# Kernel tuning notes

Hardware: AMD Instinct MI355X
Metric: run time of the kernel (lower is better)

Reference implementation:

```python
import jax, jax.numpy as jnp
import numpy as np

# SLAYER neuron / simulation constants (netParams)
THETA = 10.0      # spike threshold
TS = 1.0          # simulation timestep (ms)
TAU_SR = 10.0     # PSP (srm) time constant
TAU_REF = 1.0     # refractory time constant
SCALE_REF = 2.0   # refractory strength (in units of theta)
TAU_RHO = 1.0     # surrogate-gradient width
SCALE_RHO = 1.0   # surrogate-gradient scale
DECAY_SR = float(np.exp(-TS / TAU_SR))
DECAY_REF = float(np.exp(-TS / TAU_REF))


def psp(x):
    """Leaky-integrate PSP filter over time. x: (N, F, T) -> (N, F, T)."""
    xt = jnp.moveaxis(x, -1, 0)  # (T, N, F)
    def step(p, s):
        p = DECAY_SR * p + s
        return p, p
    _, ps = jax.lax.scan(step, jnp.zeros_like(xt[0]), xt)
    return jnp.moveaxis(ps, 0, -1)


@jax.custom_vjp
def heaviside(v):
    return (v >= 0).astype(v.dtype)

def _h_fwd(v):
    return heaviside(v), v

def _h_bwd(v, g):
    # SLAYER-style fast-sigmoid/exponential surrogate gradient
    return (g * SCALE_RHO * jnp.exp(-jnp.abs(v) / TAU_RHO),)

heaviside.defvjp(_h_fwd, _h_bwd)


def spike(u):
    """Threshold membrane potential with leaky refractory feedback.
    u: (N, F, T) -> binary spikes (N, F, T)."""
    ut = jnp.moveaxis(u, -1, 0)  # (T, N, F)
    def step(r, u_t):
        v = u_t + r                       # membrane + refractory state
        s = heaviside(v - THETA)
        r_next = DECAY_REF * (r - SCALE_REF * THETA * s)
        return r_next, s
    _, ss = jax.lax.scan(step, jnp.zeros_like(ut[0]), ut)
    return jnp.moveaxis(ss, 0, -1)


def dense(w, x):
    """Per-timestep linear layer. w: (O, F), x: (N, F, T) -> (N, O, T)."""
    return jnp.einsum('of,nft->not', w, x)


def setup_inputs() -> dict:
    key = jax.random.key(0)
    k1, k2, k3, k4, k5, k6 = jax.random.split(key, 6)
    N, T = 16, 500
    # binary spike inputs (float32 for differentiability through psp)
    xt = (jax.random.uniform(k1, (N, 156, T)) < 0.10).astype(jnp.float32)
    xv = (jax.random.uniform(k2, (N, 6300, T)) < 0.02).astype(jnp.float32)
    # dense weights (scaled so membrane potentials can cross theta=10)
    Wt = jax.random.normal(k3, (50, 156), jnp.float32) * (4.0 / np.sqrt(156))
    Wv1 = jax.random.normal(k4, (1024, 6300), jnp.float32) * (4.0 / np.sqrt(6300))
    Wv2 = jax.random.normal(k5, (10, 1024), jnp.float32) * (4.0 / np.sqrt(1024))
    Wf = jax.random.normal(k6, (20, 60), jnp.float32) * (4.0 / np.sqrt(60))
    return {"spikeInputTact": xt, "spikeInputVis": xv,
            "Wt": Wt, "Wv1": Wv1, "Wv2": Wv2, "Wf": Wf}


def reference(spikeInputTact, spikeInputVis, Wt, Wv1, Wv2, Wf):
    # tactile encoder: spike(fc1(psp(x)))
    s_tact = spike(dense(Wt, psp(spikeInputTact)))          # (N, 50, T)
    # vision encoder: two slayer dense+psp+spike stages
    sv1 = spike(dense(Wv1, psp(spikeInputVis)))             # (N, 1024, T)
    s_vis = spike(dense(Wv2, psp(sv1)))                     # (N, 10, T)
    # fuse and classify: spike(psp(fc1(cat)))
    s_all = jnp.concatenate([s_tact, s_vis], axis=1)        # (N, 60, T)
    out = spike(psp(dense(Wf, s_all)))                      # (N, 20, T)
    return out
```

## Files before the change

kernel.cpp:

```cpp
#include <hip/hip_runtime.h>
#include <stdint.h>

#define DSR   0.90483741803595952f
#define DREF  0.36787944117144233f
#define THETA 10.0f
#define REFAMP 20.0f

#define NB 16
#define TT 500
#define TP 512
#define F1 6300
#define KP 6400
#define NKS 50
#define O1 1024
#define NC 8192
#define FT 156
#define OT 50
#define O2 10
#define OF 20

typedef __attribute__((ext_vector_type(4)))  float f32x4;
typedef __attribute__((ext_vector_type(4)))  int   i32x4;
typedef __attribute__((ext_vector_type(16))) int   i32x16;

#define GLL16(g, l) __builtin_amdgcn_global_load_lds( \
    (const __attribute__((address_space(1))) void*)(g), \
    (__attribute__((address_space(3))) void*)(l), 16, 0, 0)

__global__ void __launch_bounds__(512) k_prep(const float* __restrict__ xv,
                                              const float* __restrict__ W,
                                              unsigned char* __restrict__ Bg,
                                              char* __restrict__ H0,
                                              char* __restrict__ H1) {
  __shared__ unsigned char tb[64][516];
  int bx = blockIdx.x, tid = threadIdx.x;
  if (bx < 1600) {
    int ft = bx % 100, n = bx / 100;
    int f0 = ft * 64;
    int ks = ft >> 1, half = ft & 1;
#pragma unroll
    for (int it = 0; it < 16; ++it) {
      int idx = it * 512 + tid;
      int row = idx >> 7, c4 = idx & 127;
      int f = f0 + row, t = c4 * 4;
      uchar4 b = make_uchar4(0, 0, 0, 0);
      if (f < F1) {
        if (t + 3 < TT) {
          f32x4 v = *(const f32x4*)(xv + ((size_t)n * F1 + f) * TT + t);
          b.x = (v[0] != 0.f); b.y = (v[1] != 0.f);
          b.z = (v[2] != 0.f); b.w = (v[3] != 0.f);
        } else {
#pragma unroll
          for (int j = 0; j < 4; ++j)
            if (t + j < TT) {
              float v = xv[((size_t)n * F1 + f) * TT + t + j];
              ((unsigned char*)&b)[j] = (v != 0.f);
            }
        }
      }
      *(uchar4*)&tb[row][t] = b;
    }
    __syncthreads();
    int lane = tid & 63, w = tid >> 6;
#pragma unroll 8
    for (int i = 0; i < 64; ++i) {
      int tl = w * 64 + i;
      unsigned long long mask = __ballot(tb[lane][tl] != 0);
      if (lane == 0) {
        unsigned lo = (unsigned)mask, hi = (unsigned)(mask >> 32);
        unsigned w0 = __builtin_amdgcn_perm(hi, lo, 0x05040100u);
        unsigned w1 = __builtin_amdgcn_perm(hi, lo, 0x07060302u);
        int col = n * TP + tl;
        unsigned char* g = Bg + ((size_t)ks * 8192 + col) * 16 + half * 4;
        *(unsigned*)(g) = w0;
        *(unsigned*)(g + 8) = w1;
      }
    }
  } else {
    int sb = bx - 1600;
    int o0 = sb * 4;
#pragma unroll
    for (int it = 0; it < 13; ++it) {
      int e = it * 2048 + tid * 4;
      if (e < 25600) {
        int row = e / 6400;
        int f = e - row * 6400;
        int o = o0 + row;
        float w4[4] = {0.f, 0.f, 0.f, 0.f};
        if (f < F1) {
          const f32x4 v = *(const f32x4*)(W + (size_t)o * F1 + f);
          w4[0] = v[0]; w4[1] = v[1]; w4[2] = v[2]; w4[3] = v[3];
        }
        char c0[4], c1[4];
#pragma unroll
        for (int j = 0; j < 4; ++j) {
          int wq = __float2int_rn(w4[j] * 32768.0f);
          int h0 = ((wq + 128) & 255) - 128;
          int h1 = (wq - h0) >> 8;
          c0[j] = (char)h0; c1[j] = (char)h1;
        }
        *(char4*)(H0 + (size_t)o * KP + f) = make_char4(c0[0], c0[1], c0[2], c0[3]);
        *(char4*)(H1 + (size_t)o * KP + f) = make_char4(c1[0], c1[1], c1[2], c1[3]);
      }
    }
  }
}

__global__ void __launch_bounds__(512) k_tact(const float* __restrict__ xt,
                                              const float* __restrict__ Wt,
                                              float* __restrict__ s_tact) {
  __shared__ float atv[TP * 26];
  int n = blockIdx.x >> 1, half = blockIdx.x & 1;
  int t = threadIdx.x;
  if (t < TT) {
    float acc[25];
#pragma unroll
    for (int o = 0; o < 25; ++o) acc[o] = 0.f;
    for (int f = 0; f < FT; ++f) {
      float x = xt[((size_t)n * FT + f) * TT + t];
#pragma unroll
      for (int o = 0; o < 25; ++o)
        acc[o] = fmaf(Wt[(half * 25 + o) * FT + f], x, acc[o]);
    }
#pragma unroll
    for (int o = 0; o < 25; ++o) atv[t * 26 + o] = acc[o];
  }
  __syncthreads();
  if (t < 25) {
    float p = 0.f, r = 0.f;
    float* op = s_tact + ((size_t)n * OT + half * 25 + t) * TT;
    for (int i = 0; i < TT; i += 10) {
      float u[10];
#pragma unroll
      for (int j = 0; j < 10; ++j) u[j] = atv[(i + j) * 26 + t];
#pragma unroll
      for (int j = 0; j < 10; ++j) {
        p = DSR * p + u[j];
        float v = p + r;
        bool s = (v >= THETA);
        r = DREF * (r - (s ? REFAMP : 0.f));
        op[i + j] = s ? 1.f : 0.f;
      }
    }
  }
}

__global__ void __launch_bounds__(512, 4) k_gemm(const char* __restrict__ H0,
                                                 const char* __restrict__ H1,
                                                 const unsigned char* __restrict__ Bg,
                                                 float* __restrict__ C) {
  __shared__ char A0[2][128 * 128];
  __shared__ char A1[2][128 * 128];
  int tid = threadIdx.x, bid = blockIdx.x;
  int gy = bid & 7, gx = bid >> 3;
  int wave = tid >> 6, lane = tid & 63;
  int wr = wave >> 1, wc = wave & 1;
  int l31 = lane & 31, h = lane >> 5;

  i32x16 acc0[2], acc1[2];
#pragma unroll
  for (int nn = 0; nn < 2; ++nn) { acc0[nn] = (i32x16)0; acc1[nn] = (i32x16)0; }

  size_t ga[2]; unsigned ldsa[2];
#pragma unroll
  for (int j = 0; j < 2; ++j) {
    int p = j * 512 + tid;
    int row = p >> 3;
    int src = (p & 7) ^ (row & 7);
    ga[j] = (size_t)(gy * 128 + row) * KP + src * 16;
    ldsa[j] = (unsigned)p * 16u;
  }
  const unsigned char* bp[2];
#pragma unroll
  for (int nn = 0; nn < 2; ++nn)
    bp[nn] = Bg + ((size_t)(gx * 128 + wc * 64 + nn * 32 + l31) * 16) + h * 8;

  int ra = wr * 32 + l31;
  int offA[4];
#pragma unroll
  for (int kk = 0; kk < 4; ++kk)
    offA[kk] = ra * 128 + (((kk * 2 + h) ^ (ra & 7)) * 16);

#define STAGE(ks, buf) do {                                       \
    size_t ko = (size_t)(ks) * 128;                               \
    GLL16(H0 + ga[0] + ko, (char*)&A0[buf][0] + ldsa[0]);         \
    GLL16(H0 + ga[1] + ko, (char*)&A0[buf][0] + ldsa[1]);         \
    GLL16(H1 + ga[0] + ko, (char*)&A1[buf][0] + ldsa[0]);         \
    GLL16(H1 + ga[1] + ko, (char*)&A1[buf][0] + ldsa[1]);         \
  } while (0)

#define LDB(ks, arr) do {                                         \
    _Pragma("unroll")                                             \
    for (int nn = 0; nn < 2; ++nn)                                \
      arr[nn] = *(const uint2*)(bp[nn] + (size_t)(ks) * 131072);  \
  } while (0)

#define BODY(ks, buf, bregs) do {                                               \
    if ((ks) == NKS - 1) { asm volatile("s_waitcnt vmcnt(0)" ::: "memory"); }   \
    else                 { asm volatile("s_waitcnt vmcnt(6)" ::: "memory"); }   \
    __builtin_amdgcn_sched_barrier(0);                                          \
    __builtin_amdgcn_s_barrier();                                               \
    __builtin_amdgcn_sched_barrier(0);                                          \
    _Pragma("unroll")                                                           \
    for (int kk = 0; kk < 4; ++kk) {                                            \
      i32x4 fa0 = *(const i32x4*)(&A0[buf][0] + offA[kk]);                      \
      i32x4 fa1 = *(const i32x4*)(&A1[buf][0] + offA[kk]);                      \
      i32x4 bv[2];                                                              \
      _Pragma("unroll")                                                         \
      for (int nn = 0; nn < 2; ++nn) {                                          \
        unsigned x = ((kk < 2) ? bregs[nn].x : bregs[nn].y) >> ((kk & 1) * 16); \
        x &= 0xFFFFu;                                                           \
        _Pragma("unroll")                                                       \
        for (int w = 0; w < 4; ++w) {                                           \
          unsigned nib = (x >> (4 * w)) & 0xFu;                                 \
          bv[nn][w] = (int)((nib * 0x00204081u) & 0x01010101u);                 \
        }                                                                       \
      }                                                                         \
      __builtin_amdgcn_s_setprio(1);                                            \
      _Pragma("unroll")                                                         \
      for (int nn = 0; nn < 2; ++nn) {                                          \
        acc0[nn] = __builtin_amdgcn_mfma_i32_32x32x32_i8(fa0, bv[nn], acc0[nn], 0, 0, 0); \
        acc1[nn] = __builtin_amdgcn_mfma_i32_32x32x32_i8(fa1, bv[nn], acc1[nn], 0, 0, 0); \
      }                                                                         \
      __builtin_amdgcn_s_setprio(0);                                            \
    }                                                                           \
    __builtin_amdgcn_s_barrier();                                               \
    __builtin_amdgcn_sched_barrier(0);                                          \
    if ((ks) + 2 < NKS) { STAGE((ks) + 2, buf); LDB((ks) + 2, bregs); }         \
  } while (0)

  uint2 bA[2], bB[2];
  STAGE(0, 0); LDB(0, bA);
  STAGE(1, 1); LDB(1, bB);

  for (int ks = 0; ks < NKS; ks += 2) {
    BODY(ks, 0, bA);
    BODY(ks + 1, 1, bB);
  }
#undef BODY
#undef LDB
#undef STAGE

#pragma unroll
  for (int nn = 0; nn < 2; ++nn) {
    int ob = gy * 128 + wr * 32;
    int cb = gx * 128 + wc * 64 + nn * 32 + l31;
#pragma unroll
    for (int reg = 0; reg < 16; ++reg) {
      int row = (reg & 3) + 8 * (reg >> 2) + 4 * h;
      int v = acc0[nn][reg] + (acc1[nn][reg] << 8);
      C[(size_t)(ob + row) * NC + cb] = (float)v * (1.0f / 32768.0f);
    }
  }
}

__global__ void __launch_bounds__(256) k_spk1(const float* __restrict__ C,
                                              const float* __restrict__ Wv2,
                                              float* __restrict__ a2part) {
  __shared__ float tile[128 * 65];
  __shared__ char  spkb[128 * 68];
  __shared__ float w2s[O2][64];
  int og = blockIdx.x, n = blockIdx.y;
  int tid = threadIdx.x;
  for (int i = tid; i < O2 * 64; i += 256)
    w2s[i >> 6][i & 63] = Wv2[(i >> 6) * O1 + og * 64 + (i & 63)];
  float p = 0.f, r = 0.f;
  for (int tc = 0; tc < 4; ++tc) {
#pragma unroll
    for (int i = 0; i < 8; ++i) {
      int idx = i * 256 + tid;
      int row = idx >> 5, c4 = idx & 31;
      f32x4 v = *(const f32x4*)(C + (size_t)(og * 64 + row) * NC + n * TP + tc * 128 + c4 * 4);
#pragma unroll
      for (int j = 0; j < 4; ++j) tile[(c4 * 4 + j) * 65 + row] = v[j];
    }
    __syncthreads();
    if (tid < 64) {
      float pp = p, rr = r;
      for (int i = 0; i < 128; i += 8) {
        float u[8];
#pragma unroll
        for (int j = 0; j < 8; ++j) u[j] = tile[(i + j) * 65 + tid];
#pragma unroll
        for (int j = 0; j < 8; ++j) {
          pp = DSR * pp + u[j];
          float v = pp + rr;
          bool s = (v >= THETA);
          rr = DREF * (rr - (s ? REFAMP : 0.f));
          spkb[(i + j) * 68 + tid] = s ? (char)1 : (char)0;
        }
      }
      p = pp; r = rr;
    }
    __syncthreads();
    if (tid < 128) {
      float acc[O2];
#pragma unroll
      for (int o = 0; o < O2; ++o) acc[o] = 0.f;
      for (int row = 0; row < 64; ++row) {
        float s = (spkb[tid * 68 + row] != 0) ? 1.f : 0.f;
#pragma unroll
        for (int o = 0; o < O2; ++o) acc[o] = fmaf(w2s[o][row], s, acc[o]);
      }
      int tglob = tc * 128 + tid;
#pragma unroll
      for (int o = 0; o < O2; ++o)
        a2part[(((size_t)og * NB + n) * O2 + o) * TP + tglob] = acc[o];
    }
    __syncthreads();
  }
}

__global__ void __launch_bounds__(512) k_finish(const float* __restrict__ a2part,
                                                const float* __restrict__ s_tact,
                                                const float* __restrict__ Wf,
                                                float* __restrict__ out) {
  __shared__ float u2[TP * 12];
  __shared__ float af[TP * 21];
  int n = blockIdx.x, t = threadIdx.x;
#pragma unroll
  for (int o = 0; o < O2; ++o) {
    float s = 0.f;
#pragma unroll
    for (int og = 0; og < NB; ++og)
      s += a2part[(((size_t)og * NB + n) * O2 + o) * TP + t];
    u2[t * 12 + o] = s;
  }
  __syncthreads();
  if (t < O2) {
    float p = 0.f, r = 0.f;
    for (int i = 0; i < TT; i += 10) {
      float u[10];
#pragma unroll
      for (int j = 0; j < 10; ++j) u[j] = u2[(i + j) * 12 + t];
#pragma unroll
      for (int j = 0; j < 10; ++j) {
        p = DSR * p + u[j];
        float v = p + r;
        bool s = (v >= THETA);
        r = DREF * (r - (s ? REFAMP : 0.f));
        u2[(i + j) * 12 + t] = s ? 1.f : 0.f;
      }
    }
  }
  __syncthreads();
  if (t < TT) {
    float acc[OF];
#pragma unroll
    for (int o = 0; o < OF; ++o) acc[o] = 0.f;
    for (int f = 0; f < OT; ++f) {
      float s = s_tact[((size_t)n * OT + f) * TT + t];
#pragma unroll
      for (int o = 0; o < OF; ++o) acc[o] = fmaf(Wf[o * 60 + f], s, acc[o]);
    }
#pragma unroll
    for (int f = 0; f < O2; ++f) {
      float s = u2[t * 12 + f];
#pragma unroll
      for (int o = 0; o < OF; ++o) acc[o] = fmaf(Wf[o * 60 + OT + f], s, acc[o]);
    }
#pragma unroll
    for (int o = 0; o < OF; ++o) af[t * 21 + o] = acc[o];
  }
  __syncthreads();
  if (t < OF) {
    float p = 0.f, r = 0.f;
    float* op = out + ((size_t)n * OF + t) * TT;
    for (int i = 0; i < TT; i += 10) {
      float u[10];
#pragma unroll
      for (int j = 0; j < 10; ++j) u[j] = af[(i + j) * 21 + t];
#pragma unroll
      for (int j = 0; j < 10; ++j) {
        p = DSR * p + u[j];
        float v = p + r;
        bool s = (v >= THETA);
        r = DREF * (r - (s ? REFAMP : 0.f));
        op[i + j] = s ? 1.f : 0.f;
      }
    }
  }
}

extern "C" void kernel_launch(void* const* d_in, const int* in_sizes, int n_in,
                              void* d_out, int out_size, void* d_ws, size_t ws_size,
                              hipStream_t stream) {
  (void)in_sizes; (void)n_in; (void)out_size; (void)ws_size;
  const float* xt  = (const float*)d_in[0];
  const float* xv  = (const float*)d_in[1];
  const float* Wt  = (const float*)d_in[2];
  const float* Wv1 = (const float*)d_in[3];
  const float* Wv2 = (const float*)d_in[4];
  const float* Wf  = (const float*)d_in[5];
  float* out = (float*)d_out;

  char* ws = (char*)d_ws;
  size_t off = 0;
  auto carve = [&](size_t bytes) {
    char* p = ws + off;
    off += (bytes + 255) & ~(size_t)255;
    return p;
  };
  char*          H0    = carve((size_t)O1 * KP);
  char*          H1    = carve((size_t)O1 * KP);
  unsigned char* Bg    = (unsigned char*)carve((size_t)NKS * 8192 * 16);
  float*         a1    = (float*)carve((size_t)O1 * NC * 4);
  float*         stact = (float*)carve((size_t)NB * OT * TT * 4);
  float*         a2p   = (float*)carve((size_t)NB * NB * O2 * TP * 4);

  k_prep<<<dim3(1856), dim3(512), 0, stream>>>(xv, Wv1, Bg, H0, H1);
  k_tact<<<dim3(NB * 2), dim3(512), 0, stream>>>(xt, Wt, stact);
  k_gemm<<<dim3(512), dim3(512), 0, stream>>>(H0, H1, Bg, a1);
  k_spk1<<<dim3(16, NB), dim3(256), 0, stream>>>(a1, Wv2, a2p);
  k_finish<<<dim3(NB), dim3(512), 0, stream>>>(a2p, stact, Wf, out);
}
```

Baseline: 281.7 us.

## Merge tactile encoder into spike1 kernel and stream C rows directly

Removes the separate k_tact launch by giving its work to 32 extra blocks appended to the k_spk1 grid, so the tactile path runs alongside the vision spike stage. The vision spike path now has each of 64 threads read its own C row straight from global memory with register prefetch, over the full 512-step time range. This replaces the transposed shared-memory tile and the per-chunk syncs. It saves one launch, but each thread's row reads are strided and uncoalesced, and the readout now processes four time chunks per thread.

```diff
diff --git a/kernel.cpp b/kernel.cpp
--- a/kernel.cpp
+++ b/kernel.cpp
@@ -101,45 +101,6 @@
         }
         *(char4*)(H0 + (size_t)o * KP + f) = make_char4(c0[0], c0[1], c0[2], c0[3]);
         *(char4*)(H1 + (size_t)o * KP + f) = make_char4(c1[0], c1[1], c1[2], c1[3]);
-      }
-    }
-  }
-}
-
-__global__ void __launch_bounds__(512) k_tact(const float* __restrict__ xt,
-                                              const float* __restrict__ Wt,
-                                              float* __restrict__ s_tact) {
-  __shared__ float atv[TP * 26];
-  int n = blockIdx.x >> 1, half = blockIdx.x & 1;
-  int t = threadIdx.x;
-  if (t < TT) {
-    float acc[25];
-#pragma unroll
-    for (int o = 0; o < 25; ++o) acc[o] = 0.f;
-    for (int f = 0; f < FT; ++f) {
-      float x = xt[((size_t)n * FT + f) * TT + t];
-#pragma unroll
-      for (int o = 0; o < 25; ++o)
-        acc[o] = fmaf(Wt[(half * 25 + o) * FT + f], x, acc[o]);
-    }
-#pragma unroll
-    for (int o = 0; o < 25; ++o) atv[t * 26 + o] = acc[o];
-  }
-  __syncthreads();
-  if (t < 25) {
-    float p = 0.f, r = 0.f;
-    float* op = s_tact + ((size_t)n * OT + half * 25 + t) * TT;
-    for (int i = 0; i < TT; i += 10) {
-      float u[10];
-#pragma unroll
-      for (int j = 0; j < 10; ++j) u[j] = atv[(i + j) * 26 + t];
-#pragma unroll
-      for (int j = 0; j < 10; ++j) {
-        p = DSR * p + u[j];
-        float v = p + r;
-        bool s = (v >= THETA);
-        r = DREF * (r - (s ? REFAMP : 0.f));
-        op[i + j] = s ? 1.f : 0.f;
       }
     }
   }
@@ -256,58 +217,104 @@
 
 __global__ void __launch_bounds__(256) k_spk1(const float* __restrict__ C,
                                               const float* __restrict__ Wv2,
-                                              float* __restrict__ a2part) {
-  __shared__ float tile[128 * 65];
-  __shared__ char  spkb[128 * 68];
-  __shared__ float w2s[O2][64];
-  int og = blockIdx.x, n = blockIdx.y;
-  int tid = threadIdx.x;
-  for (int i = tid; i < O2 * 64; i += 256)
-    w2s[i >> 6][i & 63] = Wv2[(i >> 6) * O1 + og * 64 + (i & 63)];
-  float p = 0.f, r = 0.f;
-  for (int tc = 0; tc < 4; ++tc) {
-#pragma unroll
-    for (int i = 0; i < 8; ++i) {
-      int idx = i * 256 + tid;
-      int row = idx >> 5, c4 = idx & 31;
-      f32x4 v = *(const f32x4*)(C + (size_t)(og * 64 + row) * NC + n * TP + tc * 128 + c4 * 4);
-#pragma unroll
-      for (int j = 0; j < 4; ++j) tile[(c4 * 4 + j) * 65 + row] = v[j];
-    }
-    __syncthreads();
+                                              float* __restrict__ a2part,
+                                              const float* __restrict__ xt,
+                                              const float* __restrict__ Wt,
+                                              float* __restrict__ s_tact) {
+  __shared__ char smem[53248];
+  int bx = blockIdx.x, tid = threadIdx.x;
+  if (bx < 256) {
+    unsigned char* spkb = (unsigned char*)smem;
+    float* w2s = (float*)(smem + 34816);
+    int og = bx >> 4, n = bx & 15;
+    for (int i = tid; i < O2 * 64; i += 256)
+      w2s[i] = Wv2[(i >> 6) * O1 + og * 64 + (i & 63)];
     if (tid < 64) {
-      float pp = p, rr = r;
-      for (int i = 0; i < 128; i += 8) {
+      const float* crow = C + (size_t)(og * 64 + tid) * NC + n * TP;
+      float p = 0.f, r = 0.f;
+      f32x4 va = *(const f32x4*)(crow);
+      f32x4 vb = *(const f32x4*)(crow + 4);
+      for (int i = 0; i < TP; i += 8) {
+        f32x4 na, nb;
+        if (i + 8 < TP) {
+          na = *(const f32x4*)(crow + i + 8);
+          nb = *(const f32x4*)(crow + i + 12);
+        }
         float u[8];
 #pragma unroll
-        for (int j = 0; j < 8; ++j) u[j] = tile[(i + j) * 65 + tid];
+        for (int j = 0; j < 4; ++j) { u[j] = va[j]; u[4 + j] = vb[j]; }
 #pragma unroll
         for (int j = 0; j < 8; ++j) {
-          pp = DSR * pp + u[j];
-          float v = pp + rr;
+          p = DSR * p + u[j];
+          float v = p + r;
           bool s = (v >= THETA);
-          rr = DREF * (rr - (s ? REFAMP : 0.f));
-          spkb[(i + j) * 68 + tid] = s ? (char)1 : (char)0;
-        }
-      }
-      p = pp; r = rr;
+          r = DREF * (r - (s ? REFAMP : 0.f));
+          spkb[(i + j) * 68 + tid] = s ? (unsigned char)1 : (unsigned char)0;
+        }
+        va = na; vb = nb;
+      }
     }
     __syncthreads();
     if (tid < 128) {
-      float acc[O2];
-#pragma unroll
-      for (int o = 0; o < O2; ++o) acc[o] = 0.f;
-      for (int row = 0; row < 64; ++row) {
-        float s = (spkb[tid * 68 + row] != 0) ? 1.f : 0.f;
-#pragma unroll
-        for (int o = 0; o < O2; ++o) acc[o] = fmaf(w2s[o][row], s, acc[o]);
-      }
-      int tglob = tc * 128 + tid;
-#pragma unroll
-      for (int o = 0; o < O2; ++o)
-        a2part[(((size_t)og * NB + n) * O2 + o) * TP + tglob] = acc[o];
+#pragma unroll
+      for (int k = 0; k < 4; ++k) {
+        int t = tid + k * 128;
+        float acc[O2];
+#pragma unroll
+        for (int o = 0; o < O2; ++o) acc[o] = 0.f;
+        for (int row = 0; row < 64; ++row) {
+          float s = (spkb[t * 68 + row] != 0) ? 1.f : 0.f;
+#pragma unroll
+          for (int o = 0; o < O2; ++o) acc[o] = fmaf(w2s[o * 64 + row], s, acc[o]);
+        }
+#pragma unroll
+        for (int o = 0; o < O2; ++o)
+          a2part[(((size_t)og * NB + n) * O2 + o) * TP + t] = acc[o];
+      }
+    }
+  } else {
+    float* atv = (float*)smem;
+    int blk = bx - 256;
+    int n = blk >> 1, half = blk & 1;
+    int t0 = tid, t1 = tid + 256;
+    {
+      float acc0[25], acc1[25];
+#pragma unroll
+      for (int o = 0; o < 25; ++o) { acc0[o] = 0.f; acc1[o] = 0.f; }
+      for (int f = 0; f < FT; ++f) {
+        float x0 = (t0 < TT) ? xt[((size_t)n * FT + f) * TT + t0] : 0.f;
+        float x1 = (t1 < TT) ? xt[((size_t)n * FT + f) * TT + t1] : 0.f;
+#pragma unroll
+        for (int o = 0; o < 25; ++o) {
+          float w = Wt[(half * 25 + o) * FT + f];
+          acc0[o] = fmaf(w, x0, acc0[o]);
+          acc1[o] = fmaf(w, x1, acc1[o]);
+        }
+      }
+#pragma unroll
+      for (int o = 0; o < 25; ++o) {
+        atv[t0 * 26 + o] = acc0[o];
+        atv[t1 * 26 + o] = acc1[o];
+      }
     }
     __syncthreads();
+    if (tid < 25) {
+      float p = 0.f, r = 0.f;
+      float* op = s_tact + ((size_t)n * OT + half * 25 + tid) * TT;
+      for (int i = 0; i < TT; i += 10) {
+        float u[10];
+#pragma unroll
+        for (int j = 0; j < 10; ++j) u[j] = atv[(i + j) * 26 + tid];
+#pragma unroll
+        for (int j = 0; j < 10; ++j) {
+          p = DSR * p + u[j];
+          float v = p + r;
+          bool s = (v >= THETA);
+          r = DREF * (r - (s ? REFAMP : 0.f));
+          op[i + j] = s ? 1.f : 0.f;
+        }
+      }
+    }
   }
 }
 
@@ -409,8 +416,7 @@
   float*         a2p   = (float*)carve((size_t)NB * NB * O2 * TP * 4);
 
   k_prep<<<dim3(1856), dim3(512), 0, stream>>>(xv, Wv1, Bg, H0, H1);
-  k_tact<<<dim3(NB * 2), dim3(512), 0, stream>>>(xt, Wt, stact);
   k_gemm<<<dim3(512), dim3(512), 0, stream>>>(H0, H1, Bg, a1);
-  k_spk1<<<dim3(16, NB), dim3(256), 0, stream>>>(a1, Wv2, a2p);
+  k_spk1<<<dim3(288), dim3(256), 0, stream>>>(a1, Wv2, a2p, xt, Wt, stact);
   k_finish<<<dim3(NB), dim3(512), 0, stream>>>(a2p, stact, Wf, out);
 }
```

New measurement: 263.2 us. -6.6%, faster.
